# Optimization experiments

Measured on AMD Instinct MI355X. Metric: run time of the kernel, lower is better.

Reference implementation:

```python
import jax, jax.numpy as jnp
import numpy as np

NUM_EXPERTS = 8
TOP_K = 2
D_MODEL = 1024
D_FF = 4096
B, S = 2, 2048


def setup_inputs() -> dict:
    key = jax.random.key(0)
    k1, k2, k3, k4 = jax.random.split(key, 4)
    scale_in = 1.0 / np.sqrt(D_MODEL)
    scale_ff = 1.0 / np.sqrt(D_FF)
    return {
        "hidden_states": jax.random.normal(k1, (B, S, D_MODEL), dtype=jnp.float32),
        "gate_w": jax.random.normal(k2, (D_MODEL, NUM_EXPERTS), dtype=jnp.float32) * scale_in,
        "w1": jax.random.normal(k3, (NUM_EXPERTS, D_MODEL, D_FF), dtype=jnp.float32) * scale_in,
        "w2": jax.random.normal(k4, (NUM_EXPERTS, D_FF, D_MODEL), dtype=jnp.float32) * scale_ff,
    }


def reference(hidden_states, gate_w, w1, w2):
    b, s, d = hidden_states.shape
    x = hidden_states.reshape(-1, d)                      # [T, d]
    gate_logits = x @ gate_w                              # [T, E]
    top_vals, top_idx = jax.lax.top_k(gate_logits, TOP_K)  # [T, K]
    # softmax over selected expert logits in fp32, cast back
    top_w = jax.nn.softmax(top_vals.astype(jnp.float32), axis=1).astype(x.dtype)
    # per-token per-expert combine weight: sum_k w[t,k] * (sel[t,k]==e)
    combine = jnp.einsum("tke,tk->te", jax.nn.one_hot(top_idx, NUM_EXPERTS, dtype=x.dtype), top_w)  # [T, E]
    # naive dense MoE: every expert over all tokens (matches torch loop)
    h = jax.nn.relu(jnp.einsum("td,edf->etf", x, w1))     # [E, T, d_ff]
    expert_out = jnp.einsum("etf,efd->etd", h, w2)        # [E, T, d]
    final = jnp.einsum("etd,te->td", expert_out, combine)  # [T, d]
    return final.reshape(b, s, d)
```

## Files before the change

### kernel.cpp

```cpp
#include <hip/hip_runtime.h>
#include <hip/hip_bf16.h>
#include <stdint.h>


#define T_TOK 4096
#define DM 1024
#define DF 4096
#define NE 8
#define BM 128
#define BN 128
#define BK 64
#define MAX_TILES 72
#define PAIR_CAP 9216

typedef __bf16 bf16x8 __attribute__((ext_vector_type(8)));
typedef float f32x4 __attribute__((ext_vector_type(4)));
typedef unsigned short ushort_t;

__device__ __forceinline__ ushort_t f2bf(float f) {
  uint32_t u = __float_as_uint(f);
  u += 0x7FFFu + ((u >> 16) & 1u);
  return (ushort_t)(u >> 16);
}
__device__ __forceinline__ float bfl(uint32_t u) { return __uint_as_float(u << 16); }
__device__ __forceinline__ float bfh(uint32_t u) { return __uint_as_float(u & 0xFFFF0000u); }

#define WT_OFF  0ull
#define XB_OFF  67108864ull
#define H_OFF   75497472ull
#define PO_OFF  159383552ull
#define RT_OFF  201326592ull
#define RO_COUNTS   0
#define RO_OFFSETS  32
#define RO_CURSORS  64
#define RO_NTILES   96
#define RO_TILE_E   128
#define RO_TILE_S   448
#define RO_TILE_R   768
#define RO_PTOK     1088
#define RO_PW       37952
#define RO_TOPI     74816
#define RO_TOPW     107584
#define RO_PIDX     140352
#define RT_BYTES    173120ull
#define WS_NEEDED   (RT_OFF + RT_BYTES)

__device__ __forceinline__ int xcd_work(int b, int live) {
  int k = b & 7, j = b >> 3;
  int q = live >> 3, r = live & 7;
  int cnt = q + (k < r ? 1 : 0);
  if (j >= cnt) return -1;
  int start = k * q + (k < r ? k : r);
  return start + j;
}

__global__ void gate_kernel(const float* __restrict__ x, const float* __restrict__ gw,
                            int* __restrict__ counts, int* __restrict__ topi,
                            float* __restrict__ topw, ushort_t* __restrict__ xb) {
  int wave = threadIdx.x >> 6;
  int lane = threadIdx.x & 63;
  int t = blockIdx.x * 4 + wave;
  const float* xr = x + (size_t)t * DM;
  ushort_t* xbr = xb + (size_t)t * DM;
  float acc[NE];
#pragma unroll
  for (int e = 0; e < NE; ++e) acc[e] = 0.f;
  for (int d = lane; d < DM; d += 64) {
    float xv = xr[d];
    xbr[d] = f2bf(xv);
    const float* g = gw + (size_t)d * NE;
#pragma unroll
    for (int e = 0; e < NE; ++e) acc[e] += xv * g[e];
  }
#pragma unroll
  for (int off = 32; off > 0; off >>= 1) {
#pragma unroll
    for (int e = 0; e < NE; ++e) acc[e] += __shfl_xor(acc[e], off, 64);
  }
  if (lane == 0) {
    int i0 = 0; float v0 = acc[0];
#pragma unroll
    for (int e = 1; e < NE; ++e) if (acc[e] > v0) { v0 = acc[e]; i0 = e; }
    int i1 = -1; float v1 = -1e30f;
#pragma unroll
    for (int e = 0; e < NE; ++e) if (e != i0 && acc[e] > v1) { v1 = acc[e]; i1 = e; }
    float e1 = expf(v1 - v0);
    float w0 = 1.f / (1.f + e1);
    float w1 = e1 / (1.f + e1);
    topi[t * 2] = i0; topi[t * 2 + 1] = i1;
    topw[t * 2] = w0; topw[t * 2 + 1] = w1;
    atomicAdd(&counts[i0], 1);
    atomicAdd(&counts[i1], 1);
  }
}

__global__ void scan_kernel(const int* __restrict__ counts, int* __restrict__ offsets,
                            int* __restrict__ cursors, int* __restrict__ n_tiles,
                            int* __restrict__ tile_e, int* __restrict__ tile_s,
                            int* __restrict__ tile_r) {
  if (threadIdx.x == 0) {
    int off = 0, nt = 0;
    for (int e = 0; e < NE; ++e) {
      offsets[e] = off;
      cursors[e] = 0;
      int c = counts[e];
      for (int m0 = 0; m0 < c; m0 += BM) {
        tile_e[nt] = e;
        tile_s[nt] = off + m0;
        tile_r[nt] = (c - m0 < BM) ? (c - m0) : BM;
        ++nt;
      }
      off += ((c + BM - 1) / BM) * BM;
    }
    *n_tiles = nt;
  }
}

__global__ void scatter_kernel(const int* __restrict__ topi, const float* __restrict__ topw,
                               const int* __restrict__ offsets, int* __restrict__ cursors,
                               int* __restrict__ ptok, float* __restrict__ pw,
                               int* __restrict__ pidx) {
  int t = blockIdx.x * 256 + threadIdx.x;
  if (t >= T_TOK) return;
#pragma unroll
  for (int k = 0; k < 2; ++k) {
    int e = topi[t * 2 + k];
    int pos = atomicAdd(&cursors[e], 1);
    int p = offsets[e] + pos;
    ptok[p] = t;
    pw[p] = topw[t * 2 + k];
    pidx[t * 2 + k] = p;
  }
}

__global__ void transpose_convert(const float* __restrict__ src, ushort_t* __restrict__ dst,
                                  int R, int C) {
  __shared__ ushort_t tile[64][136];
  int e = blockIdx.z;
  src += (size_t)e * R * C;
  dst += (size_t)e * R * C;
  int c0 = blockIdx.x * 64, r0 = blockIdx.y * 128;
  int tr = threadIdx.x >> 4;
  int tc = (threadIdx.x & 15) << 2;
#pragma unroll
  for (int i = 0; i < 8; ++i) {
    int r = i * 16 + tr;
    float4 v = *(const float4*)&src[(size_t)(r0 + r) * C + c0 + tc];
    tile[tc + 0][r] = f2bf(v.x);
    tile[tc + 1][r] = f2bf(v.y);
    tile[tc + 2][r] = f2bf(v.z);
    tile[tc + 3][r] = f2bf(v.w);
  }
  __syncthreads();
  int cr = threadIdx.x >> 5;
  int rg = (threadIdx.x & 31) << 2;
#pragma unroll
  for (int j = 0; j < 8; ++j) {
    int c = j * 8 + cr;
    ushort4 o = { tile[c][rg], tile[c][rg + 1], tile[c][rg + 2], tile[c][rg + 3] };
    *(ushort4*)&dst[(size_t)(c0 + c) * R + r0 + rg] = o;
  }
}


#define GLD(srcp, dstp)                                                        \
  __builtin_amdgcn_global_load_lds(                                            \
      (const __attribute__((address_space(1))) void*)(srcp),                   \
      (__attribute__((address_space(3))) void*)(dstp), 16, 0, 0)

__device__ __forceinline__ void gemm_core(
    ushort_t* As, ushort_t* Bs,
    const ushort_t* const (&a_sp)[4], const ushort_t* const (&b_sp)[4],
    int NT, int wid, int lane, f32x4 (&acc)[4][4]) {
  int fr = lane & 15, ch = lane >> 4, sw = lane & 7;
  int k0s = (ch ^ sw) * 8;
  int k1s = ((ch + 4) ^ sw) * 8;
  int m_off = (wid >> 1) * 64, n_off = (wid & 1) * 64;
  int abase = (m_off + fr) * 64;
  int bbase = (n_off + fr) * 64;

  for (int t = 0; t < NT; ++t) {
    int k0 = t * BK;
#pragma unroll
    for (int j = 0; j < 4; ++j) {
      GLD(a_sp[j] + k0, As + (wid * 4 + j) * 512);
      GLD(b_sp[j] + k0, Bs + (wid * 4 + j) * 512);
    }
    asm volatile("s_waitcnt vmcnt(0)" ::: "memory");
    __syncthreads();

#pragma unroll
    for (int kx = 0; kx < 2; ++kx) {
      int ks = kx ? k1s : k0s;
      bf16x8 af[4], bf[4];
#pragma unroll
      for (int mi = 0; mi < 4; ++mi) af[mi] = *(const bf16x8*)&As[abase + mi * 1024 + ks];
#pragma unroll
      for (int ni = 0; ni < 4; ++ni) bf[ni] = *(const bf16x8*)&Bs[bbase + ni * 1024 + ks];
#pragma unroll
      for (int mi = 0; mi < 4; ++mi)
#pragma unroll
        for (int ni = 0; ni < 4; ++ni)
          acc[mi][ni] = __builtin_amdgcn_mfma_f32_16x16x32_bf16(af[mi], bf[ni], acc[mi][ni], 0, 0, 0);
    }
    __syncthreads();
  }
}

__global__ __launch_bounds__(256, 4) void gemm1_kernel(
    const ushort_t* __restrict__ xb, const ushort_t* __restrict__ w1t,
    ushort_t* __restrict__ h,
    const int* __restrict__ n_tiles, const int* __restrict__ tile_e,
    const int* __restrict__ tile_s, const int* __restrict__ tile_r,
    const int* __restrict__ ptok) {
  int work = xcd_work(blockIdx.x, *n_tiles * (DF / BN));
  if (work < 0) return;
  int tile = work >> 5;
  int n0 = (work & 31) * BN;
  int e = tile_e[tile], p0 = tile_s[tile], rows = tile_r[tile];

  __shared__ ushort_t As[BM * BK];
  __shared__ ushort_t Bs[BN * BK];
  int tid = threadIdx.x, wid = tid >> 6, lane = tid & 63;
  int lr = lane >> 3;
  int swc = (lane & 7) ^ (lr & 7);

  const ushort_t* a_sp[4];
  const ushort_t* b_sp[4];
#pragma unroll
  for (int j = 0; j < 4; ++j) {
    int r = wid * 32 + j * 8 + lr;
    int tok = (r < rows) ? ptok[p0 + r] : 0;
    a_sp[j] = xb + (size_t)tok * DM + swc * 8;
    b_sp[j] = w1t + ((size_t)e * DF + n0 + r) * DM + swc * 8;
  }

  f32x4 acc[4][4] = {};
  gemm_core(As, Bs, a_sp, b_sp, DM / BK, wid, lane, acc);

  int m_off = (wid >> 1) * 64, n_off = (wid & 1) * 64;
  int col = lane & 15, rq = (lane >> 4) * 4;
#pragma unroll
  for (int mi = 0; mi < 4; ++mi)
#pragma unroll
    for (int r = 0; r < 4; ++r) {
      int m = m_off + mi * 16 + rq + r;
      bool valid = m < rows;
      size_t rowoff = (size_t)(p0 + m) * DF + n0 + n_off;
#pragma unroll
      for (int ni = 0; ni < 4; ++ni) {
        float v = acc[mi][ni][r];
        v = valid ? (v > 0.f ? v : 0.f) : 0.f;
        h[rowoff + ni * 16 + col] = f2bf(v);
      }
    }
}

__global__ __launch_bounds__(256, 4) void gemm2_kernel(
    const ushort_t* __restrict__ h, const ushort_t* __restrict__ w2t,
    ushort_t* __restrict__ po,
    const int* __restrict__ n_tiles, const int* __restrict__ tile_e,
    const int* __restrict__ tile_s, const int* __restrict__ tile_r,
    const float* __restrict__ pw) {
  int work = xcd_work(blockIdx.x, *n_tiles * (DM / BN) * 2);
  if (work < 0) return;
  int tile = work >> 4;
  int sub = work & 15;
  int n0 = (sub >> 1) * BN;
  int kh = sub & 1;
  int kof = kh * (DF / 2);
  int e = tile_e[tile], p0 = tile_s[tile], rows = tile_r[tile];

  __shared__ ushort_t As[BM * BK];
  __shared__ ushort_t Bs[BN * BK];
  int tid = threadIdx.x, wid = tid >> 6, lane = tid & 63;
  int lr = lane >> 3;
  int swc = (lane & 7) ^ (lr & 7);

  const ushort_t* a_sp[4];
  const ushort_t* b_sp[4];
#pragma unroll
  for (int j = 0; j < 4; ++j) {
    int r = wid * 32 + j * 8 + lr;
    a_sp[j] = h + (size_t)(p0 + r) * DF + kof + swc * 8;
    b_sp[j] = w2t + ((size_t)e * DM + n0 + r) * DF + kof + swc * 8;
  }

  f32x4 acc[4][4] = {};
  gemm_core(As, Bs, a_sp, b_sp, DF / (2 * BK), wid, lane, acc);

  ushort_t* pod = po + (size_t)kh * PAIR_CAP * DM;
  int m_off = (wid >> 1) * 64, n_off = (wid & 1) * 64;
  int col = lane & 15, rq = (lane >> 4) * 4;
#pragma unroll
  for (int mi = 0; mi < 4; ++mi)
#pragma unroll
    for (int r = 0; r < 4; ++r) {
      int m = m_off + mi * 16 + rq + r;
      if (m < rows) {
        int p = p0 + m;
        float w = pw[p];
        size_t o = (size_t)p * DM + n0 + n_off;
#pragma unroll
        for (int ni = 0; ni < 4; ++ni)
          pod[o + ni * 16 + col] = f2bf(w * acc[mi][ni][r]);
      }
    }
}

__global__ void combine_kernel(const ushort_t* __restrict__ po, const int* __restrict__ pidx,
                               float* __restrict__ out) {
  int idx = blockIdx.x * 256 + threadIdx.x;
  int t = idx >> 7;
  int d8 = (idx & 127) << 3;
  int pa = pidx[t * 2], pb = pidx[t * 2 + 1];
  const size_t HS = (size_t)PAIR_CAP * DM;
  size_t oa = (size_t)pa * DM + d8, ob = (size_t)pb * DM + d8;
  uint4 va0 = *(const uint4*)&po[oa];
  uint4 vb0 = *(const uint4*)&po[ob];
  uint4 va1 = *(const uint4*)&po[HS + oa];
  uint4 vb1 = *(const uint4*)&po[HS + ob];
  const uint32_t* A0 = (const uint32_t*)&va0;
  const uint32_t* B0 = (const uint32_t*)&vb0;
  const uint32_t* A1 = (const uint32_t*)&va1;
  const uint32_t* B1 = (const uint32_t*)&vb1;
  float r[8];
#pragma unroll
  for (int w = 0; w < 4; ++w) {
    r[2 * w]     = bfl(A0[w]) + bfl(B0[w]) + bfl(A1[w]) + bfl(B1[w]);
    r[2 * w + 1] = bfh(A0[w]) + bfh(B0[w]) + bfh(A1[w]) + bfh(B1[w]);
  }
  float4 o0 = { r[0], r[1], r[2], r[3] };
  float4 o1 = { r[4], r[5], r[6], r[7] };
  size_t ob2 = (size_t)t * DM + d8;
  *(float4*)&out[ob2] = o0;
  *(float4*)&out[ob2 + 4] = o1;
}

extern "C" void kernel_launch(void* const* d_in, const int* in_sizes, int n_in,
                              void* d_out, int out_size, void* d_ws, size_t ws_size,
                              hipStream_t stream) {
  const float* x  = (const float*)d_in[0];
  const float* gw = (const float*)d_in[1];
  const float* w1 = (const float*)d_in[2];
  const float* w2 = (const float*)d_in[3];
  float* out = (float*)d_out;
  char* ws = (char*)d_ws;
  if (ws_size < WS_NEEDED) return;

  ushort_t* wt  = (ushort_t*)(ws + WT_OFF);
  ushort_t* xb  = (ushort_t*)(ws + XB_OFF);
  ushort_t* h   = (ushort_t*)(ws + H_OFF);
  ushort_t* po  = (ushort_t*)(ws + PO_OFF);
  char* rt = ws + RT_OFF;
  int*   counts  = (int*)(rt + RO_COUNTS);
  int*   offsets = (int*)(rt + RO_OFFSETS);
  int*   cursors = (int*)(rt + RO_CURSORS);
  int*   n_tiles = (int*)(rt + RO_NTILES);
  int*   tile_e  = (int*)(rt + RO_TILE_E);
  int*   tile_s  = (int*)(rt + RO_TILE_S);
  int*   tile_r  = (int*)(rt + RO_TILE_R);
  int*   ptok    = (int*)(rt + RO_PTOK);
  float* pw      = (float*)(rt + RO_PW);
  int*   topi    = (int*)(rt + RO_TOPI);
  float* topw    = (float*)(rt + RO_TOPW);
  int*   pidx    = (int*)(rt + RO_PIDX);

  hipMemsetAsync(rt, 0, 128, stream);

  hipLaunchKernelGGL(gate_kernel, dim3(T_TOK / 4), dim3(256), 0, stream,
                     x, gw, counts, topi, topw, xb);
  hipLaunchKernelGGL(scan_kernel, dim3(1), dim3(64), 0, stream,
                     counts, offsets, cursors, n_tiles, tile_e, tile_s, tile_r);
  hipLaunchKernelGGL(scatter_kernel, dim3(T_TOK / 256), dim3(256), 0, stream,
                     topi, topw, offsets, cursors, ptok, pw, pidx);
  hipLaunchKernelGGL(transpose_convert, dim3(DF / 64, DM / 128, NE), dim3(256), 0, stream,
                     w1, wt, DM, DF);
  hipLaunchKernelGGL(gemm1_kernel, dim3(MAX_TILES * (DF / BN)), dim3(256), 0, stream,
                     xb, wt, h, n_tiles, tile_e, tile_s, tile_r, ptok);
  hipLaunchKernelGGL(transpose_convert, dim3(DM / 64, DF / 128, NE), dim3(256), 0, stream,
                     w2, wt, DF, DM);
  hipLaunchKernelGGL(gemm2_kernel, dim3(MAX_TILES * (DM / BN) * 2), dim3(256), 0, stream,
                     h, wt, po, n_tiles, tile_e, tile_s, tile_r, pw);
  hipLaunchKernelGGL(combine_kernel, dim3((T_TOK * DM / 8) / 256), dim3(256), 0, stream,
                     po, pidx, out);
}
```

Before: 419.6 us.

## Enlarge expert GEMM row tile to 256 with 128x64 per-wave subtiles

Doubles the M tile of both expert GEMMs from 128 to 256 rows, so each wave computes a 128x64 output block with 8x4 MFMA accumulators. This raises arithmetic intensity per loaded weight tile and halves the number of tiles that reread expert weights. The routing buffers, tile capacity and pair capacity are resized to match. In exchange, padding waste grows for partially filled expert tiles, register pressure doubles (launch bounds drop to 2 blocks per SM), and fewer blocks are available for parallelism.

```diff
diff --git a/kernel.cpp b/kernel.cpp
--- a/kernel.cpp
+++ b/kernel.cpp
@@ -7,11 +7,11 @@
 #define DM 1024
 #define DF 4096
 #define NE 8
-#define BM 128
+#define BM 256
 #define BN 128
 #define BK 64
-#define MAX_TILES 72
-#define PAIR_CAP 9216
+#define MAX_TILES 40
+#define PAIR_CAP 10240
 
 typedef __bf16 bf16x8 __attribute__((ext_vector_type(8)));
 typedef float f32x4 __attribute__((ext_vector_type(4)));
@@ -35,14 +35,14 @@
 #define RO_CURSORS  64
 #define RO_NTILES   96
 #define RO_TILE_E   128
-#define RO_TILE_S   448
-#define RO_TILE_R   768
-#define RO_PTOK     1088
-#define RO_PW       37952
-#define RO_TOPI     74816
-#define RO_TOPW     107584
-#define RO_PIDX     140352
-#define RT_BYTES    173120ull
+#define RO_TILE_S   320
+#define RO_TILE_R   512
+#define RO_PTOK     1024
+#define RO_PW       41984
+#define RO_TOPI     82944
+#define RO_TOPW     115712
+#define RO_PIDX     148480
+#define RT_BYTES    181248ull
 #define WS_NEEDED   (RT_OFF + RT_BYTES)
 
 __device__ __forceinline__ int xcd_work(int b, int live) {
@@ -170,44 +170,43 @@
 
 __device__ __forceinline__ void gemm_core(
     ushort_t* As, ushort_t* Bs,
-    const ushort_t* const (&a_sp)[4], const ushort_t* const (&b_sp)[4],
-    int NT, int wid, int lane, f32x4 (&acc)[4][4]) {
+    const ushort_t* const (&a_sp)[8], const ushort_t* const (&b_sp)[4],
+    int NT, int wid, int lane, f32x4 (&acc)[8][4]) {
   int fr = lane & 15, ch = lane >> 4, sw = lane & 7;
   int k0s = (ch ^ sw) * 8;
   int k1s = ((ch + 4) ^ sw) * 8;
-  int m_off = (wid >> 1) * 64, n_off = (wid & 1) * 64;
-  int abase = (m_off + fr) * 64;
-  int bbase = (n_off + fr) * 64;
+  int wr = wid >> 1, wc = wid & 1;
+  int abase = (wr * 128 + fr) * 64;
+  int bbase = (wc * 64 + fr) * 64;
 
   for (int t = 0; t < NT; ++t) {
     int k0 = t * BK;
 #pragma unroll
-    for (int j = 0; j < 4; ++j) {
-      GLD(a_sp[j] + k0, As + (wid * 4 + j) * 512);
-      GLD(b_sp[j] + k0, Bs + (wid * 4 + j) * 512);
-    }
+    for (int j = 0; j < 8; ++j) GLD(a_sp[j] + k0, As + (wid * 8 + j) * 512);
+#pragma unroll
+    for (int j = 0; j < 4; ++j) GLD(b_sp[j] + k0, Bs + (wid * 4 + j) * 512);
     asm volatile("s_waitcnt vmcnt(0)" ::: "memory");
     __syncthreads();
 
 #pragma unroll
     for (int kx = 0; kx < 2; ++kx) {
       int ks = kx ? k1s : k0s;
-      bf16x8 af[4], bf[4];
-#pragma unroll
-      for (int mi = 0; mi < 4; ++mi) af[mi] = *(const bf16x8*)&As[abase + mi * 1024 + ks];
+      bf16x8 bf[4];
 #pragma unroll
       for (int ni = 0; ni < 4; ++ni) bf[ni] = *(const bf16x8*)&Bs[bbase + ni * 1024 + ks];
 #pragma unroll
-      for (int mi = 0; mi < 4; ++mi)
+      for (int mi = 0; mi < 8; ++mi) {
+        bf16x8 af = *(const bf16x8*)&As[abase + mi * 1024 + ks];
 #pragma unroll
         for (int ni = 0; ni < 4; ++ni)
-          acc[mi][ni] = __builtin_amdgcn_mfma_f32_16x16x32_bf16(af[mi], bf[ni], acc[mi][ni], 0, 0, 0);
+          acc[mi][ni] = __builtin_amdgcn_mfma_f32_16x16x32_bf16(af, bf[ni], acc[mi][ni], 0, 0, 0);
+      }
     }
     __syncthreads();
   }
 }
 
-__global__ __launch_bounds__(256, 4) void gemm1_kernel(
+__global__ __launch_bounds__(256, 2) void gemm1_kernel(
     const ushort_t* __restrict__ xb, const ushort_t* __restrict__ w1t,
     ushort_t* __restrict__ h,
     const int* __restrict__ n_tiles, const int* __restrict__ tile_e,
@@ -225,28 +224,32 @@
   int lr = lane >> 3;
   int swc = (lane & 7) ^ (lr & 7);
 
-  const ushort_t* a_sp[4];
+  const ushort_t* a_sp[8];
   const ushort_t* b_sp[4];
+#pragma unroll
+  for (int j = 0; j < 8; ++j) {
+    int r = wid * 64 + j * 8 + lr;
+    int tok = (r < rows) ? ptok[p0 + r] : 0;
+    a_sp[j] = xb + (size_t)tok * DM + swc * 8;
+  }
 #pragma unroll
   for (int j = 0; j < 4; ++j) {
     int r = wid * 32 + j * 8 + lr;
-    int tok = (r < rows) ? ptok[p0 + r] : 0;
-    a_sp[j] = xb + (size_t)tok * DM + swc * 8;
     b_sp[j] = w1t + ((size_t)e * DF + n0 + r) * DM + swc * 8;
   }
 
-  f32x4 acc[4][4] = {};
+  f32x4 acc[8][4] = {};
   gemm_core(As, Bs, a_sp, b_sp, DM / BK, wid, lane, acc);
 
-  int m_off = (wid >> 1) * 64, n_off = (wid & 1) * 64;
+  int wr = wid >> 1, wc = wid & 1;
   int col = lane & 15, rq = (lane >> 4) * 4;
 #pragma unroll
-  for (int mi = 0; mi < 4; ++mi)
+  for (int mi = 0; mi < 8; ++mi)
 #pragma unroll
     for (int r = 0; r < 4; ++r) {
-      int m = m_off + mi * 16 + rq + r;
+      int m = wr * 128 + mi * 16 + rq + r;
       bool valid = m < rows;
-      size_t rowoff = (size_t)(p0 + m) * DF + n0 + n_off;
+      size_t rowoff = (size_t)(p0 + m) * DF + n0 + wc * 64;
 #pragma unroll
       for (int ni = 0; ni < 4; ++ni) {
         float v = acc[mi][ni][r];
@@ -256,7 +259,7 @@
     }
 }
 
-__global__ __launch_bounds__(256, 4) void gemm2_kernel(
+__global__ __launch_bounds__(256, 2) void gemm2_kernel(
     const ushort_t* __restrict__ h, const ushort_t* __restrict__ w2t,
     ushort_t* __restrict__ po,
     const int* __restrict__ n_tiles, const int* __restrict__ tile_e,
@@ -277,30 +280,34 @@
   int lr = lane >> 3;
   int swc = (lane & 7) ^ (lr & 7);
 
-  const ushort_t* a_sp[4];
+  const ushort_t* a_sp[8];
   const ushort_t* b_sp[4];
+#pragma unroll
+  for (int j = 0; j < 8; ++j) {
+    int r = wid * 64 + j * 8 + lr;
+    a_sp[j] = h + (size_t)(p0 + r) * DF + kof + swc * 8;
+  }
 #pragma unroll
   for (int j = 0; j < 4; ++j) {
     int r = wid * 32 + j * 8 + lr;
-    a_sp[j] = h + (size_t)(p0 + r) * DF + kof + swc * 8;
     b_sp[j] = w2t + ((size_t)e * DM + n0 + r) * DF + kof + swc * 8;
   }
 
-  f32x4 acc[4][4] = {};
+  f32x4 acc[8][4] = {};
   gemm_core(As, Bs, a_sp, b_sp, DF / (2 * BK), wid, lane, acc);
 
   ushort_t* pod = po + (size_t)kh * PAIR_CAP * DM;
-  int m_off = (wid >> 1) * 64, n_off = (wid & 1) * 64;
+  int wr = wid >> 1, wc = wid & 1;
   int col = lane & 15, rq = (lane >> 4) * 4;
 #pragma unroll
-  for (int mi = 0; mi < 4; ++mi)
+  for (int mi = 0; mi < 8; ++mi)
 #pragma unroll
     for (int r = 0; r < 4; ++r) {
-      int m = m_off + mi * 16 + rq + r;
+      int m = wr * 128 + mi * 16 + rq + r;
       if (m < rows) {
         int p = p0 + m;
         float w = pw[p];
-        size_t o = (size_t)p * DM + n0 + n_off;
+        size_t o = (size_t)p * DM + n0 + wc * 64;
 #pragma unroll
         for (int ni = 0; ni < 4; ++ni)
           pod[o + ni * 16 + col] = f2bf(w * acc[mi][ni][r]);
```

Measured after the change: 457.6 us. 1.09x slower.
